# Performance work log

Measured on AMD Instinct MI355X. Metric: run time of the kernel, lower is better.

Reference implementation:

```python
import jax, jax.numpy as jnp
import numpy as np
import math

EMBED_DIM = 1024
NUM_HEADS = 16
HEAD_DIM = EMBED_DIM // NUM_HEADS
CQ = 256  # chunksize_q
CK = 256  # chunksize_k
L = 2048
B = 4


def setup_inputs() -> dict:
    key = jax.random.key(0)
    ks = jax.random.split(key, 7)
    E = EMBED_DIM
    # xavier_uniform bound for (3E, E): sqrt(6/(3E+E))
    bound = math.sqrt(6.0 / (3 * E + E))
    in_proj_weight = jax.random.uniform(ks[3], (3 * E, E), jnp.float32, -bound, bound)
    in_proj_bias = jnp.zeros((3 * E,), jnp.float32)
    # nn.Linear default init (kaiming uniform ~ U(-1/sqrt(E), 1/sqrt(E)))
    wb = 1.0 / math.sqrt(E)
    out_w = jax.random.uniform(ks[4], (E, E), jnp.float32, -wb, wb)
    out_b = jnp.zeros((E,), jnp.float32)
    return {
        "q": jax.random.normal(ks[0], (L, B, E), jnp.float32),
        "k": jax.random.normal(ks[1], (L, B, E), jnp.float32),
        "v": jax.random.normal(ks[2], (L, B, E), jnp.float32),
        "in_proj_weight": in_proj_weight,
        "in_proj_bias": in_proj_bias,
        "out_w": out_w,
        "out_b": out_b,
    }


def _chunked_attention(q, k, v):
    # q: (BH, Lq, d), k/v: (BH, Lk, d). Online-softmax over k-chunks,
    # vectorized over the chunk grid (same math as the python loops).
    BH, Lq, d = q.shape
    Lk = k.shape[1]
    nq, nk = Lq // CQ, Lk // CK
    q = q / math.sqrt(HEAD_DIM)
    qc = q.reshape(BH, nq, CQ, d)
    kc = k.reshape(BH, nk, CK, d)
    vc = v.reshape(BH, nk, CK, d)
    # scores per (q-chunk, k-chunk) pair: (BH, nq, nk, CQ, CK)
    s = jnp.einsum('bqid,bkjd->bqkij', qc, kc)
    m = jax.lax.stop_gradient(jnp.max(s, axis=-1, keepdims=True))  # detached chunk max
    e = jnp.exp(s - m)
    row_sum = e.sum(axis=-1)                                # (BH, nq, nk, CQ)
    vals = jnp.einsum('bqkij,bkjd->bqkid', e, vc)           # (BH, nq, nk, CQ, d)
    m = m[..., 0]                                           # (BH, nq, nk, CQ)
    gmax = jnp.max(m, axis=2, keepdims=True)                # global max over k-chunks
    diff = jnp.exp(m - gmax)
    all_vals = (vals * diff[..., None]).sum(axis=2)         # (BH, nq, CQ, d)
    all_w = (row_sum * diff).sum(axis=2)[..., None]         # (BH, nq, CQ, 1)
    out = all_vals / all_w
    return out.reshape(BH, Lq, d)


def reference(q, k, v, in_proj_weight, in_proj_bias, out_w, out_b):
    E, H, hd = EMBED_DIM, NUM_HEADS, HEAD_DIM
    l, b, _ = q.shape
    lk = k.shape[0]
    w_q, w_k, w_v = jnp.split(in_proj_weight, 3, axis=0)
    b_q, b_k, b_v = jnp.split(in_proj_bias, 3, axis=0)
    qp = q @ w_q.T + b_q
    kp = k @ w_k.T + b_k
    vp = v @ w_v.T + b_v
    # (L, B, E) -> (B*H, L, hd)
    qp = qp.reshape(l, b * H, hd).transpose(1, 0, 2)
    kp = kp.reshape(lk, b * H, hd).transpose(1, 0, 2)
    vp = vp.reshape(lk, b * H, hd).transpose(1, 0, 2)
    attn = _chunked_attention(qp, kp, vp)                   # (B*H, L, hd)
    attn = attn.transpose(1, 0, 2).reshape(l, b, E)
    return attn @ out_w.T + out_b
```

## Files before the change

kernel.cpp:

```cpp
#include <hip/hip_runtime.h>

typedef unsigned short u16;
typedef short bf16x8 __attribute__((ext_vector_type(8)));
typedef float f32x4 __attribute__((ext_vector_type(4)));
typedef unsigned u32x2 __attribute__((ext_vector_type(2)));

#define MFMA16(a, b, c) __builtin_amdgcn_mfma_f32_16x16x32_bf16(a, b, c, 0, 0, 0)

static constexpr int L_ = 2048, B_ = 4, E_ = 1024, H_ = 16, HD_ = 64;
static constexpr int M_ = L_ * B_;
static constexpr int BH_ = B_ * H_;
static constexpr size_t NA = (size_t)M_ * E_;
#define QSCALE 0.18033688f

__device__ __forceinline__ void gload16(const void* g, void* l) {
  __builtin_amdgcn_global_load_lds((const __attribute__((address_space(1))) void*)g,
                                   (__attribute__((address_space(3))) void*)l, 16, 0, 0);
}

__device__ __forceinline__ u16 f2bf(float f) {
  union { float f; unsigned u; } v; v.f = f;
  unsigned r = v.u + 0x7fffu + ((v.u >> 16) & 1u);
  return (u16)(r >> 16);
}

__device__ __forceinline__ unsigned pkbf(float a, float b) {
#if __has_builtin(__builtin_amdgcn_cvt_pk_bf16_f32)
  auto r = __builtin_amdgcn_cvt_pk_bf16_f32(a, b);
  unsigned u; __builtin_memcpy(&u, &r, 4); return u;
#else
  return (unsigned)f2bf(a) | ((unsigned)f2bf(b) << 16);
#endif
}

__device__ __forceinline__ float fexp2(float x) {
#if __has_builtin(__builtin_amdgcn_exp2f)
  return __builtin_amdgcn_exp2f(x);
#else
  return exp2f(x);
#endif
}

__global__ __launch_bounds__(256) void cvt_all(
    const float* __restrict__ q, const float* __restrict__ k, const float* __restrict__ v,
    const float* __restrict__ w, const float* __restrict__ ow,
    u16* __restrict__ qb, u16* __restrict__ kb, u16* __restrict__ vb,
    u16* __restrict__ wbf, u16* __restrict__ owbf) {
  const size_t idx = ((size_t)blockIdx.x * 256 + threadIdx.x) * 8;
  const float* s; u16* d; size_t off;
  if (idx < NA) { s = q; d = qb; off = idx; }
  else if (idx < 2 * NA) { s = k; d = kb; off = idx - NA; }
  else if (idx < 3 * NA) { s = v; d = vb; off = idx - 2 * NA; }
  else if (idx < 3 * NA + (size_t)3 * E_ * E_) { s = w; d = wbf; off = idx - 3 * NA; }
  else { s = ow; d = owbf; off = idx - 3 * NA - (size_t)3 * E_ * E_; }
  const float4 a = *(const float4*)(s + off);
  const float4 b = *(const float4*)(s + off + 4);
  uint4 r;
  r.x = pkbf(a.x, a.y); r.y = pkbf(a.z, a.w);
  r.z = pkbf(b.x, b.y); r.w = pkbf(b.z, b.w);
  *(uint4*)(d + off) = r;
}

__global__ __launch_bounds__(256) void gemm_qkv(
    const u16* __restrict__ Aq, const u16* __restrict__ Ak, const u16* __restrict__ Av,
    const u16* __restrict__ Wbf, const float* __restrict__ bias,
    u16* __restrict__ oq, u16* __restrict__ ok, u16* __restrict__ ov) {
  __shared__ __align__(16) u16 As[128][64];
  __shared__ __align__(16) u16 Bs[128][64];
  const int t = threadIdx.x, wave = t >> 6, lane = t & 63, quad = lane >> 4, l15 = lane & 15;
  const int n0 = blockIdx.x * 128, m0 = blockIdx.y * 128, z = blockIdx.z;
  const u16* A = (z == 0) ? Aq : (z == 1 ? Ak : Av);
  const u16* Wz = Wbf + (size_t)z * E_ * E_;
  const float* bz = bias + z * E_;
  const int wm = (wave >> 1) * 64, wn = (wave & 1) * 64;

  const f32x4 vzero = {0.f, 0.f, 0.f, 0.f};
  f32x4 acc[4][4];
#pragma unroll
  for (int i = 0; i < 4; ++i)
#pragma unroll
    for (int j = 0; j < 4; ++j) acc[i][j] = vzero;

  for (int kk = 0; kk < E_; kk += 64) {
#pragma unroll
    for (int i = 0; i < 4; ++i) {
      const int c0 = (i * 4 + wave) * 64;
      const int c = c0 + lane;
      const int r = c >> 3;
      const int p = (c & 7) ^ (r & 7);
      gload16(A + (size_t)(m0 + r) * E_ + kk + p * 8, (u16*)As + c0 * 8);
      gload16(Wz + (size_t)(n0 + r) * E_ + kk + p * 8, (u16*)Bs + c0 * 8);
    }
    __syncthreads();
#pragma unroll
    for (int ks = 0; ks < 2; ++ks) {
      bf16x8 af[4], bfr[4];
#pragma unroll
      for (int x = 0; x < 4; ++x) {
        const int ra = wm + x * 16 + l15;
        af[x] = *(const bf16x8*)&As[ra][(((ks * 4 + quad)) ^ (ra & 7)) * 8];
        const int rb = wn + x * 16 + l15;
        bfr[x] = *(const bf16x8*)&Bs[rb][(((ks * 4 + quad)) ^ (rb & 7)) * 8];
      }
#pragma unroll
      for (int mi = 0; mi < 4; ++mi)
#pragma unroll
        for (int ni = 0; ni < 4; ++ni)
          acc[mi][ni] = MFMA16(af[mi], bfr[ni], acc[mi][ni]);
    }
    __syncthreads();
  }

#pragma unroll
  for (int ni = 0; ni < 4; ++ni) {
    const int n = n0 + wn + ni * 16 + l15;
    const float bv = bz[n];
#pragma unroll
    for (int mi = 0; mi < 4; ++mi) {
#pragma unroll
      for (int r = 0; r < 4; ++r) {
        const int m = m0 + wm + mi * 16 + quad * 4 + r;
        const float val = acc[mi][ni][r] + bv;
        const int l = m >> 2, bb = m & 3, h = n >> 6, d = n & 63;
        const int s = bb * H_ + h;
        if (z == 0) {
          oq[(size_t)s * (L_ * HD_) + (size_t)l * HD_ + d] = f2bf(val * QSCALE);
        } else if (z == 1) {
          ok[(size_t)s * (L_ * HD_) + (size_t)l * HD_ + d] = f2bf(val);
        } else {
          ov[((size_t)s * HD_ + d) * L_ + l] = f2bf(val);
        }
      }
    }
  }
}

__global__ __launch_bounds__(256) void gemm_out(
    const u16* __restrict__ A, const u16* __restrict__ Wbf,
    const float* __restrict__ bias, float* __restrict__ out) {
  __shared__ __align__(16) u16 As[128][64];
  __shared__ __align__(16) u16 Bs[128][64];
  const int t = threadIdx.x, wave = t >> 6, lane = t & 63, quad = lane >> 4, l15 = lane & 15;
  const int n0 = blockIdx.x * 128, m0 = blockIdx.y * 128;
  const int wm = (wave >> 1) * 64, wn = (wave & 1) * 64;

  const f32x4 vzero = {0.f, 0.f, 0.f, 0.f};
  f32x4 acc[4][4];
#pragma unroll
  for (int i = 0; i < 4; ++i)
#pragma unroll
    for (int j = 0; j < 4; ++j) acc[i][j] = vzero;

  for (int kk = 0; kk < E_; kk += 64) {
#pragma unroll
    for (int i = 0; i < 4; ++i) {
      const int c0 = (i * 4 + wave) * 64;
      const int c = c0 + lane;
      const int r = c >> 3;
      const int p = (c & 7) ^ (r & 7);
      gload16(A + (size_t)(m0 + r) * E_ + kk + p * 8, (u16*)As + c0 * 8);
      gload16(Wbf + (size_t)(n0 + r) * E_ + kk + p * 8, (u16*)Bs + c0 * 8);
    }
    __syncthreads();
#pragma unroll
    for (int ks = 0; ks < 2; ++ks) {
      bf16x8 af[4], bfr[4];
#pragma unroll
      for (int x = 0; x < 4; ++x) {
        const int ra = wm + x * 16 + l15;
        af[x] = *(const bf16x8*)&As[ra][(((ks * 4 + quad)) ^ (ra & 7)) * 8];
        const int rb = wn + x * 16 + l15;
        bfr[x] = *(const bf16x8*)&Bs[rb][(((ks * 4 + quad)) ^ (rb & 7)) * 8];
      }
#pragma unroll
      for (int mi = 0; mi < 4; ++mi)
#pragma unroll
        for (int ni = 0; ni < 4; ++ni)
          acc[mi][ni] = MFMA16(af[mi], bfr[ni], acc[mi][ni]);
    }
    __syncthreads();
  }

#pragma unroll
  for (int ni = 0; ni < 4; ++ni) {
    const int n = n0 + wn + ni * 16 + l15;
    const float bv = bias[n];
#pragma unroll
    for (int mi = 0; mi < 4; ++mi) {
#pragma unroll
      for (int r = 0; r < 4; ++r) {
        const int m = m0 + wm + mi * 16 + quad * 4 + r;
        out[(size_t)m * E_ + n] = acc[mi][ni][r] + bv;
      }
    }
  }
}

__global__ __launch_bounds__(256, 4) void attn_fused(
    const u16* __restrict__ Q, const u16* __restrict__ K,
    const u16* __restrict__ Vt, u16* __restrict__ O) {
  __shared__ __align__(16) u16 Ks[64][64];
  __shared__ __align__(16) u16 Vs[64][64];
  __shared__ __align__(16) u16 Ps[4][2048];
  const int t = threadIdx.x, wave = t >> 6, lane = t & 63, quad = lane >> 4, l15 = lane & 15;
  const int id = blockIdx.y * 16 + blockIdx.x;
  const int nid = (id & 7) * 128 + (id >> 3);
  const int bh = nid >> 4, q0 = (nid & 15) * 128;
  const u16* Qb = Q + (size_t)bh * L_ * HD_;
  const u16* Kb = K + (size_t)bh * L_ * HD_;
  const u16* Vb = Vt + (size_t)bh * HD_ * L_;
  u16* Pw = Ps[wave];

  bf16x8 qf[2][2];
#pragma unroll
  for (int g = 0; g < 2; ++g) {
    const int qrow = q0 + wave * 32 + g * 16 + l15;
    qf[g][0] = *(const bf16x8*)(Qb + (size_t)qrow * HD_ + quad * 8);
    qf[g][1] = *(const bf16x8*)(Qb + (size_t)qrow * HD_ + 32 + quad * 8);
  }

  bf16x8 vone;
#pragma unroll
  for (int j = 0; j < 8; ++j) vone[j] = (short)0x3F80;

  const f32x4 vzero = {0.f, 0.f, 0.f, 0.f};
  f32x4 oacc[2][4];
  f32x4 dacc[2];
#pragma unroll
  for (int g = 0; g < 2; ++g) {
    dacc[g] = vzero;
#pragma unroll
    for (int di = 0; di < 4; ++di) oacc[g][di] = vzero;
  }

  const int sigma = (l15 & 7) ^ ((l15 >> 2) & 2);
  u16* Pwb = Pw + l15 * 64 + (quad & 1) * 4;
  const int qh = quad >> 1;

  for (int j0 = 0; j0 < L_; j0 += 64) {
#pragma unroll
    for (int i = 0; i < 2; ++i) {
      const int c0 = (i * 4 + wave) * 64;
      const int c = c0 + lane;
      const int r = c >> 3, p = (c & 7) ^ (r & 7);
      gload16(Kb + (size_t)(j0 + r) * HD_ + p * 8, (u16*)Ks + c0 * 8);
      gload16(Vb + (size_t)r * L_ + j0 + p * 8, (u16*)Vs + c0 * 8);
    }
    __syncthreads();

    __builtin_amdgcn_s_setprio(1);
#pragma unroll
    for (int ni = 0; ni < 4; ++ni) {
      const int row = ni * 16 + l15;
      const bf16x8 k0 = *(const bf16x8*)&Ks[row][(quad ^ (row & 7)) * 8];
      const bf16x8 k1 = *(const bf16x8*)&Ks[row][((4 + quad) ^ (row & 7)) * 8];
      f32x4 s0 = vzero, s1 = vzero;
      s0 = MFMA16(k0, qf[0][0], s0);
      s0 = MFMA16(k1, qf[0][1], s0);
      s1 = MFMA16(k0, qf[1][0], s1);
      s1 = MFMA16(k1, qf[1][1], s1);
      const int go = ((2 * ni + qh) ^ sigma) << 3;
      {
        const float p0 = fexp2(s0[0]), p1 = fexp2(s0[1]);
        const float p2 = fexp2(s0[2]), p3 = fexp2(s0[3]);
        u32x2 pv; pv.x = pkbf(p0, p1); pv.y = pkbf(p2, p3);
        *(u32x2*)(Pwb + go) = pv;
      }
      {
        const float p0 = fexp2(s1[0]), p1 = fexp2(s1[1]);
        const float p2 = fexp2(s1[2]), p3 = fexp2(s1[3]);
        u32x2 pv; pv.x = pkbf(p0, p1); pv.y = pkbf(p2, p3);
        *(u32x2*)(Pwb + 1024 + go) = pv;
      }
    }

#pragma unroll
    for (int s2 = 0; s2 < 2; ++s2) {
      const int go = ((s2 * 4 + quad) ^ sigma) << 3;
      const bf16x8 pa0 = *(const bf16x8*)(Pw + l15 * 64 + go);
      const bf16x8 pa1 = *(const bf16x8*)(Pw + 1024 + l15 * 64 + go);
      dacc[0] = MFMA16(pa0, vone, dacc[0]);
      dacc[1] = MFMA16(pa1, vone, dacc[1]);
#pragma unroll
      for (int di = 0; di < 4; ++di) {
        const int row = di * 16 + l15;
        const bf16x8 vb = *(const bf16x8*)&Vs[row][((s2 * 4 + quad) ^ (row & 7)) * 8];
        oacc[0][di] = MFMA16(pa0, vb, oacc[0][di]);
        oacc[1][di] = MFMA16(pa1, vb, oacc[1][di]);
      }
    }
    __builtin_amdgcn_s_setprio(0);
    __syncthreads();
  }

  const int b = bh >> 4, h = bh & 15;
#pragma unroll
  for (int g = 0; g < 2; ++g) {
#pragma unroll
    for (int r = 0; r < 4; ++r) {
      const float inv = 1.f / dacc[g][r];
      const int l = q0 + wave * 32 + g * 16 + quad * 4 + r;
#pragma unroll
      for (int di = 0; di < 4; ++di) {
        const int e = h * 64 + di * 16 + l15;
        O[((size_t)l * B_ + b) * E_ + e] = f2bf(oacc[g][di][r] * inv);
      }
    }
  }
}

extern "C" void kernel_launch(void* const* d_in, const int* in_sizes, int n_in,
                              void* d_out, int out_size, void* d_ws, size_t ws_size,
                              hipStream_t stream) {
  const float* q = (const float*)d_in[0];
  const float* k = (const float*)d_in[1];
  const float* v = (const float*)d_in[2];
  const float* w = (const float*)d_in[3];
  const float* bqkv = (const float*)d_in[4];
  const float* ow = (const float*)d_in[5];
  const float* ob = (const float*)d_in[6];

  u16* qb = (u16*)d_ws;
  u16* kb = qb + NA;
  u16* vb = kb + NA;
  u16* qs = vb + NA;
  u16* ks = qs + NA;
  u16* vt = ks + NA;
  u16* wbf = vt + NA;
  u16* owbf = wbf + (size_t)3 * E_ * E_;
  u16* obuf = qb;

  cvt_all<<<dim3(14336), 256, 0, stream>>>(q, k, v, w, ow, qb, kb, vb, wbf, owbf);
  gemm_qkv<<<dim3(E_ / 128, M_ / 128, 3), 256, 0, stream>>>(qb, kb, vb, wbf, bqkv, qs, ks, vt);
  attn_fused<<<dim3(16, BH_), 256, 0, stream>>>(qs, ks, vt, obuf);
  gemm_out<<<dim3(E_ / 128, M_ / 128), 256, 0, stream>>>(obuf, owbf, ob, (float*)d_out);
}
```

Before: 355.8 us.

## Double-buffer LDS tiles in QKV GEMM and attention kernels

Adds a second LDS buffer for the A/B tiles in the QKV projection GEMM and the K/V tiles in the fused attention kernel, and issues global-to-LDS loads for the next tile before computing on the current one. This is meant to hide global load latency behind MFMA work instead of stalling at a barrier each iteration. It doubles LDS use per block, which may lower occupancy. It also depends on the existing end-of-loop barrier plus the async load completing before the next read.

```diff
diff --git a/kernel.cpp b/kernel.cpp
--- a/kernel.cpp
+++ b/kernel.cpp
@@ -65,8 +65,8 @@
     const u16* __restrict__ Aq, const u16* __restrict__ Ak, const u16* __restrict__ Av,
     const u16* __restrict__ Wbf, const float* __restrict__ bias,
     u16* __restrict__ oq, u16* __restrict__ ok, u16* __restrict__ ov) {
-  __shared__ __align__(16) u16 As[128][64];
-  __shared__ __align__(16) u16 Bs[128][64];
+  __shared__ __align__(16) u16 As[2][128][64];
+  __shared__ __align__(16) u16 Bs[2][128][64];
   const int t = threadIdx.x, wave = t >> 6, lane = t & 63, quad = lane >> 4, l15 = lane & 15;
   const int n0 = blockIdx.x * 128, m0 = blockIdx.y * 128, z = blockIdx.z;
   const u16* A = (z == 0) ? Aq : (z == 1 ? Ak : Av);
@@ -81,26 +81,33 @@
 #pragma unroll
     for (int j = 0; j < 4; ++j) acc[i][j] = vzero;
 
-  for (int kk = 0; kk < E_; kk += 64) {
+  auto stage = [&](int b, int kk) {
 #pragma unroll
     for (int i = 0; i < 4; ++i) {
       const int c0 = (i * 4 + wave) * 64;
       const int c = c0 + lane;
       const int r = c >> 3;
       const int p = (c & 7) ^ (r & 7);
-      gload16(A + (size_t)(m0 + r) * E_ + kk + p * 8, (u16*)As + c0 * 8);
-      gload16(Wz + (size_t)(n0 + r) * E_ + kk + p * 8, (u16*)Bs + c0 * 8);
-    }
-    __syncthreads();
+      gload16(A + (size_t)(m0 + r) * E_ + kk + p * 8, (u16*)As[b] + c0 * 8);
+      gload16(Wz + (size_t)(n0 + r) * E_ + kk + p * 8, (u16*)Bs[b] + c0 * 8);
+    }
+  };
+
+  stage(0, 0);
+  __syncthreads();
+
+  for (int it = 0; it < 16; ++it) {
+    const int cur = it & 1;
+    if (it < 15) stage(cur ^ 1, (it + 1) * 64);
 #pragma unroll
     for (int ks = 0; ks < 2; ++ks) {
       bf16x8 af[4], bfr[4];
 #pragma unroll
       for (int x = 0; x < 4; ++x) {
         const int ra = wm + x * 16 + l15;
-        af[x] = *(const bf16x8*)&As[ra][(((ks * 4 + quad)) ^ (ra & 7)) * 8];
+        af[x] = *(const bf16x8*)&As[cur][ra][(((ks * 4 + quad)) ^ (ra & 7)) * 8];
         const int rb = wn + x * 16 + l15;
-        bfr[x] = *(const bf16x8*)&Bs[rb][(((ks * 4 + quad)) ^ (rb & 7)) * 8];
+        bfr[x] = *(const bf16x8*)&Bs[cur][rb][(((ks * 4 + quad)) ^ (rb & 7)) * 8];
       }
 #pragma unroll
       for (int mi = 0; mi < 4; ++mi)
@@ -199,8 +206,8 @@
 __global__ __launch_bounds__(256, 4) void attn_fused(
     const u16* __restrict__ Q, const u16* __restrict__ K,
     const u16* __restrict__ Vt, u16* __restrict__ O) {
-  __shared__ __align__(16) u16 Ks[64][64];
-  __shared__ __align__(16) u16 Vs[64][64];
+  __shared__ __align__(16) u16 Ks[2][64][64];
+  __shared__ __align__(16) u16 Vs[2][64][64];
   __shared__ __align__(16) u16 Ps[4][2048];
   const int t = threadIdx.x, wave = t >> 6, lane = t & 63, quad = lane >> 4, l15 = lane & 15;
   const int id = blockIdx.y * 16 + blockIdx.x;
@@ -237,23 +244,31 @@
   u16* Pwb = Pw + l15 * 64 + (quad & 1) * 4;
   const int qh = quad >> 1;
 
-  for (int j0 = 0; j0 < L_; j0 += 64) {
+  auto stage = [&](int b, int j0) {
 #pragma unroll
     for (int i = 0; i < 2; ++i) {
       const int c0 = (i * 4 + wave) * 64;
       const int c = c0 + lane;
       const int r = c >> 3, p = (c & 7) ^ (r & 7);
-      gload16(Kb + (size_t)(j0 + r) * HD_ + p * 8, (u16*)Ks + c0 * 8);
-      gload16(Vb + (size_t)r * L_ + j0 + p * 8, (u16*)Vs + c0 * 8);
-    }
-    __syncthreads();
+      gload16(Kb + (size_t)(j0 + r) * HD_ + p * 8, (u16*)Ks[b] + c0 * 8);
+      gload16(Vb + (size_t)r * L_ + j0 + p * 8, (u16*)Vs[b] + c0 * 8);
+    }
+  };
+
+  stage(0, 0);
+  __syncthreads();
+
+  const int NT = L_ / 64;
+  for (int it = 0; it < NT; ++it) {
+    const int cur = it & 1;
+    if (it + 1 < NT) stage(cur ^ 1, (it + 1) * 64);
 
     __builtin_amdgcn_s_setprio(1);
 #pragma unroll
     for (int ni = 0; ni < 4; ++ni) {
       const int row = ni * 16 + l15;
-      const bf16x8 k0 = *(const bf16x8*)&Ks[row][(quad ^ (row & 7)) * 8];
-      const bf16x8 k1 = *(const bf16x8*)&Ks[row][((4 + quad) ^ (row & 7)) * 8];
+      const bf16x8 k0 = *(const bf16x8*)&Ks[cur][row][(quad ^ (row & 7)) * 8];
+      const bf16x8 k1 = *(const bf16x8*)&Ks[cur][row][((4 + quad) ^ (row & 7)) * 8];
       f32x4 s0 = vzero, s1 = vzero;
       s0 = MFMA16(k0, qf[0][0], s0);
       s0 = MFMA16(k1, qf[0][1], s0);
@@ -284,7 +299,7 @@
 #pragma unroll
       for (int di = 0; di < 4; ++di) {
         const int row = di * 16 + l15;
-        const bf16x8 vb = *(const bf16x8*)&Vs[row][((s2 * 4 + quad) ^ (row & 7)) * 8];
+        const bf16x8 vb = *(const bf16x8*)&Vs[cur][row][((s2 * 4 + quad) ^ (row & 7)) * 8];
         oacc[0][di] = MFMA16(pa0, vb, oacc[0][di]);
         oacc[1][di] = MFMA16(pa1, vb, oacc[1][di]);
       }
```

Result: slower. 372.8 us (+4.8%).
